# Optimization experiments

Hardware: AMD Instinct MI355X
Metric: run time of the kernel (lower is better)

Reference implementation:

```python
import jax, jax.numpy as jnp
import numpy as np

PATCH_SIZES = [4, 8, 12, 24]
SEQ_LEN = 336
D_MODEL = 512
BATCH = 256
N_EXPERTS = 4


def _build_gates():
    """Balanced top-2 routing: sample b -> experts (b%E, (b+1)%E). NNZ=512, 128 per expert."""
    rng = np.random.default_rng(0)
    gates = np.zeros((BATCH, N_EXPERTS), np.float32)
    for b in range(BATCH):
        e1, e2 = b % N_EXPERTS, (b + 1) % N_EXPERTS
        g = rng.uniform(0.1, 1.0, size=2).astype(np.float32)
        g = g / g.sum()
        gates[b, e1] = g[0]
        gates[b, e2] = g[1]
    nz = np.argwhere(gates > 0)                       # [NNZ, 2], batch-major (row-major)
    order = np.argsort(nz[:, 1], kind='stable')       # stable sort by expert -> batch order within expert
    return gates, nz[order, 0].astype(np.int64), nz[order, 1].astype(np.int64)


def setup_inputs() -> dict:
    key = jax.random.key(0)
    gates_np, batch_index, expert_index = _build_gates()
    counts = [int((expert_index == i).sum()) for i in range(N_EXPERTS)]  # 128 each
    keys = jax.random.split(key, 16)
    inp = {}
    for i, p in enumerate(PATCH_SIZES):
        L = SEQ_LEN // p
        inp[f'xs{i}'] = jax.random.normal(keys[i], (counts[i], L, D_MODEL), jnp.float32)
        inp[f'W{i}'] = jax.random.normal(keys[4 + i], (p * D_MODEL, D_MODEL), jnp.float32) * 0.02
        inp[f'b{i}'] = jnp.zeros((p * D_MODEL,), jnp.float32)
    inp['gates'] = jnp.asarray(gates_np)
    inp['Wp'] = jax.random.normal(keys[8], (D_MODEL, D_MODEL), jnp.float32) * 0.02
    inp['bp'] = jnp.zeros((D_MODEL,), jnp.float32)
    inp['batch_index'] = jnp.asarray(batch_index)
    inp['expert_index'] = jnp.asarray(expert_index)
    return inp


def reference(xs0, xs1, xs2, xs3, gates, W0, b0, W1, b1, W2, b2, W3, b3, Wp, bp,
              batch_index, expert_index):
    xs = [xs0, xs1, xs2, xs3]
    Ws = [(W0, b0), (W1, b1), (W2, b2), (W3, b3)]
    outs = []
    for x, (W, b), p in zip(xs, Ws, PATCH_SIZES):
        h = jnp.einsum('nld,pd->nlp', x, W) + b       # [N_i, L_i, P*D]
        n, l, _ = h.shape
        h = h.reshape(n, l * p, D_MODEL)[:, :SEQ_LEN]  # [N_i, seq_len, D]
        outs.append(h)
    stitched = jnp.concatenate(outs, axis=0)           # [NNZ, seq_len, D], expert-major
    proj = jnp.einsum('nld,ed->nle', stitched, Wp) + bp
    nonzero_gates = gates[batch_index, expert_index]   # [NNZ]
    proj = proj * nonzero_gates[:, None, None]
    combined = jnp.zeros((gates.shape[0], SEQ_LEN, D_MODEL), proj.dtype)
    combined = combined.at[batch_index].add(proj)      # gated scatter-combine
    return combined
```

## Files before the change

kernel.cpp:

```cpp
#include <hip/hip_runtime.h>
#include <stdint.h>

typedef __bf16 bf16_t;
typedef bf16_t bf16x8 __attribute__((ext_vector_type(8)));
typedef float f32x4 __attribute__((ext_vector_type(4)));
typedef unsigned short u16x8 __attribute__((ext_vector_type(8)));

#define KDIM 512

__device__ __forceinline__ unsigned short f2bf(float f) {
  unsigned int u = __float_as_uint(f);
  u = (u + 0x7FFFu + ((u >> 16) & 1u)) >> 16;
  return (unsigned short)u;
}

struct PrepArgs {
  const float *s0, *s1, *s2, *s3, *s4;
  unsigned short *d0, *d1, *d2, *d3, *d4;
  const float *w0, *w1, *w2, *w3;
  unsigned short *t0, *t1, *t2, *t3;
  const float *b0, *b1, *b2, *b3;
  const float *Wp, *bp;
  float *bf;
};
__device__ __forceinline__ void cvt8(const float* s, unsigned short* d, int i) {
  const float4* sp = (const float4*)s;
  float4 a = sp[2 * (size_t)i], b = sp[2 * (size_t)i + 1];
  u16x8 r;
  r[0] = f2bf(a.x); r[1] = f2bf(a.y); r[2] = f2bf(a.z); r[3] = f2bf(a.w);
  r[4] = f2bf(b.x); r[5] = f2bf(b.y); r[6] = f2bf(b.z); r[7] = f2bf(b.w);
  *(u16x8*)(d + (size_t)8 * i) = r;
}
__global__ __launch_bounds__(256) void prep_all(PrepArgs a) {
  __shared__ float tile[64][65];
  int bid = blockIdx.x;
  int t = threadIdx.x;
  if (bid < 48) {
    int jg = bid;
    int e, base;
    if (jg < 4)       { e = 0; base = 0; }
    else if (jg < 12) { e = 1; base = 4; }
    else if (jg < 24) { e = 2; base = 12; }
    else              { e = 3; base = 24; }
    const float* b = e == 0 ? a.b0 : e == 1 ? a.b1 : e == 2 ? a.b2 : a.b3;
    int jl = jg - base;
    const float4* br4 = (const float4*)(b + (size_t)jl * 512);
#pragma unroll
    for (int oo = 0; oo < 2; ++oo) {
      int o = t + oo * 256;
      const float4* wr4 = (const float4*)(a.Wp + (size_t)o * 512);
      float sx = 0.f, sy = 0.f, sz = 0.f, sw = 0.f;
#pragma unroll 4
      for (int i = 0; i < 128; ++i) {
        float4 wv = wr4[i], bv = br4[i];
        sx += wv.x * bv.x; sy += wv.y * bv.y; sz += wv.z * bv.z; sw += wv.w * bv.w;
      }
      a.bf[(size_t)jg * 512 + o] = a.bp[o] + ((sx + sy) + (sz + sw));
    }
  } else if (bid < 3120) {
    int r = bid - 48;
    int e, base, P;
    if (r < 256)       { e = 0; base = 0;    P = 4; }
    else if (r < 768)  { e = 1; base = 256;  P = 8; }
    else if (r < 1536) { e = 2; base = 768;  P = 12; }
    else               { e = 3; base = 1536; P = 24; }
    const float* W = e == 0 ? a.w0 : e == 1 ? a.w1 : e == 2 ? a.w2 : a.w3;
    unsigned short* Wt = e == 0 ? a.t0 : e == 1 ? a.t1 : e == 2 ? a.t2 : a.t3;
    r -= base;
    int qb = r % (P * 8), db = r / (P * 8);
    int q0 = qb * 64, d0 = db * 64;
    int c4 = t & 15, rgrp = t >> 4;
#pragma unroll
    for (int i = 0; i < 4; ++i) {
      int row = rgrp + i * 16;
      float4 v = *(const float4*)&W[(size_t)(q0 + row) * 512 + d0 + c4 * 4];
      tile[row][c4 * 4 + 0] = v.x; tile[row][c4 * 4 + 1] = v.y;
      tile[row][c4 * 4 + 2] = v.z; tile[row][c4 * 4 + 3] = v.w;
    }
    __syncthreads();
    int j = q0 >> 9, e0 = q0 & 511;
    size_t obase = (size_t)j * 262144 + (size_t)d0 * 512 + e0;
#pragma unroll
    for (int it = 0; it < 2; ++it) {
      int pair = it * 256 + t;
      int dd = pair >> 3, ch = pair & 7;
      u16x8 o8;
#pragma unroll
      for (int k = 0; k < 8; ++k) o8[k] = f2bf(tile[ch * 8 + k][dd]);
      *(u16x8*)&Wt[obase + (size_t)dd * 512 + ch * 8] = o8;
    }
  } else {
    int i = (bid - 3120) * 256 + t;
    if (i < 688128)       cvt8(a.s0, a.d0, i);
    else if (i < 1032192) cvt8(a.s1, a.d1, i - 688128);
    else if (i < 1261568) cvt8(a.s2, a.d2, i - 1032192);
    else if (i < 1376256) cvt8(a.s3, a.d3, i - 1261568);
    else                  cvt8(a.s4, a.d4, i - 1376256);
  }
}

__device__ __forceinline__ void gload_lds16(const unsigned short* g, unsigned short* l) {
  __builtin_amdgcn_global_load_lds(
      (const __attribute__((address_space(1))) void*)g,
      (__attribute__((address_space(3))) void*)l, 16, 0, 0);
}

__device__ __forceinline__ void stage32(const unsigned short* __restrict__ g,
                                        char* ldsOp, int tid, int kt) {
  int rlo = tid >> 2;
  int c = (tid & 3) ^ ((tid >> 3) & 3);
#pragma unroll
  for (int i = 0; i < 2; ++i) {
    int row = i * 64 + rlo;
    gload_lds16(g + (size_t)row * KDIM + kt * 32 + c * 8,
                (unsigned short*)(ldsOp + i * 4096 + tid * 16));
  }
}
__device__ __forceinline__ bf16x8 lds_frag32(const char* op, int r, int c16) {
  return *(const bf16x8*)(op + r * 64 + ((c16 ^ ((r >> 1) & 3)) << 4));
}

__device__ __forceinline__ void gemm128_k512(
    const unsigned short* __restrict__ Ag, const unsigned short* __restrict__ Bg,
    char* lds, int tid, f32x4 acc[4][4]) {
  int lane = tid & 63, w = tid >> 6;
  int wr0 = (w >> 1) * 64, wc0 = (w & 1) * 64;
  int c16 = lane >> 4, rl = lane & 15;
  stage32(Ag, lds, tid, 0);
  stage32(Bg, lds + 8192, tid, 0);
  stage32(Ag, lds + 16384, tid, 1);
  stage32(Bg, lds + 16384 + 8192, tid, 1);
#pragma unroll
  for (int s = 0; s < 16; ++s) {
    if (s < 15) asm volatile("s_waitcnt vmcnt(4)\n\ts_barrier" ::: "memory");
    else        asm volatile("s_waitcnt vmcnt(0)\n\ts_barrier" ::: "memory");
    char* cur = lds + (s % 3) * 16384;
    if (s + 2 < 16) {
      char* nxt = lds + ((s + 2) % 3) * 16384;
      stage32(Ag, nxt, tid, s + 2);
      stage32(Bg, nxt + 8192, tid, s + 2);
    }
    bf16x8 av[4], bv[4];
#pragma unroll
    for (int f = 0; f < 4; ++f) {
      av[f] = lds_frag32(cur, wr0 + f * 16 + rl, c16);
      bv[f] = lds_frag32(cur + 8192, wc0 + f * 16 + rl, c16);
    }
    __builtin_amdgcn_s_setprio(1);
#pragma unroll
    for (int fi = 0; fi < 4; ++fi)
#pragma unroll
      for (int fj = 0; fj < 4; ++fj)
        acc[fi][fj] = __builtin_amdgcn_mfma_f32_16x16x32_bf16(av[fi], bv[fj], acc[fi][fj], 0, 0, 0);
    __builtin_amdgcn_s_setprio(0);
  }
}

struct FuseArgs {
  const unsigned short *wt0, *wt1, *wt2, *wt3;
  unsigned short *wf0, *wf1, *wf2, *wf3;
};
__global__ __launch_bounds__(256, 3) void fuse_all(const unsigned short* __restrict__ Wpb, FuseArgs a) {
  __shared__ __align__(16) char lds[49152];
  int bid = blockIdx.x;
  int e, base, P;
  if (bid < 64)       { e = 0; base = 0;   P = 4; }
  else if (bid < 192) { e = 1; base = 64;  P = 8; }
  else if (bid < 384) { e = 2; base = 192; P = 12; }
  else                { e = 3; base = 384; P = 24; }
  const unsigned short* WtB = e == 0 ? a.wt0 : e == 1 ? a.wt1 : e == 2 ? a.wt2 : a.wt3;
  unsigned short* Wf = e == 0 ? a.wf0 : e == 1 ? a.wf1 : e == 2 ? a.wf2 : a.wf3;
  int r = bid - base;
  int tileM = r % (4 * P), tileN = r / (4 * P);
  int tid = threadIdx.x;
  int lane = tid & 63, w = tid >> 6;
  int wr0 = (w >> 1) * 64, wc0 = (w & 1) * 64;
  int j = (tileM * 128) >> 9;
  const unsigned short* Ag = Wpb + (size_t)((tileM * 128) & 511) * 512;
  const unsigned short* Bg = WtB + (size_t)j * 262144 + (size_t)(tileN * 128) * 512;
  f32x4 acc[4][4] = {};
  gemm128_k512(Ag, Bg, lds, tid, acc);
#pragma unroll
  for (int fi = 0; fi < 4; ++fi)
#pragma unroll
    for (int fj = 0; fj < 4; ++fj) {
      int col = tileN * 128 + wc0 + fj * 16 + (lane & 15);
#pragma unroll
      for (int r2 = 0; r2 < 4; ++r2) {
        int m = tileM * 128 + wr0 + fi * 16 + (lane >> 4) * 4 + r2;
        Wf[(size_t)m * 512 + col] = f2bf(acc[fi][fj][r2]);
      }
    }
}

template <int L, int P, int EXPERT, bool SLICE_M, bool STORE>
__device__ __forceinline__ void expert_body(
    const unsigned short* __restrict__ A, const unsigned short* __restrict__ Wf,
    const float* __restrict__ bf, const float* __restrict__ gates,
    const int* __restrict__ bidx, float* __restrict__ out, char* lds, int bid, int tid) {
  constexpr int TM = L;
  constexpr int TN = 4 * P;
  constexpr int EBASE = 128 * EXPERT;
  int xcd = bid & 7, pos = bid >> 3;
  int lin = xcd * (TM * TN / 8) + pos;
  int tileM, tileN;
  if (SLICE_M) { tileM = lin / TN; tileN = lin % TN; }
  else         { tileN = lin / TM; tileM = lin % TM; }

  int lane = tid & 63, w = tid >> 6;
  int wr0 = (w >> 1) * 64, wc0 = (w & 1) * 64;
  const unsigned short* Ag = A + (size_t)tileM * 128 * KDIM;
  const unsigned short* Bg = Wf + (size_t)tileN * 128 * KDIM;
  f32x4 acc[4][4] = {};
  gemm128_k512(Ag, Bg, lds, tid, acc);

  int j = tileN >> 2;
  int obase = (tileN & 3) * 128;
  float bv[4];
  int ocol[4];
#pragma unroll
  for (int fj = 0; fj < 4; ++fj) {
    ocol[fj] = obase + wc0 + fj * 16 + (lane & 15);
    bv[fj] = bf[(j << 9) + ocol[fj]];
  }
#pragma unroll
  for (int fi = 0; fi < 4; ++fi) {
    int m0 = tileM * 128 + wr0 + fi * 16 + (lane >> 4) * 4;
    int n = m0 / L, li = m0 - n * L;
    float* rp[4]; float gg[4];
#pragma unroll
    for (int r = 0; r < 4; ++r) {
      if (li == L) { li = 0; ++n; }
      int b = bidx[EBASE + n];
      gg[r] = gates[b * 4 + EXPERT];
      rp[r] = out + ((size_t)b * 336 + li * P + j) * 512;
      ++li;
    }
    float old[4][4];
    if (!STORE) {
#pragma unroll
      for (int r = 0; r < 4; ++r)
#pragma unroll
        for (int fj = 0; fj < 4; ++fj) old[r][fj] = rp[r][ocol[fj]];
    }
#pragma unroll
    for (int r = 0; r < 4; ++r)
#pragma unroll
      for (int fj = 0; fj < 4; ++fj) {
        float v = gg[r] * (acc[fi][fj][r] + bv[fj]);
        if (!STORE) v += old[r][fj];
        rp[r][ocol[fj]] = v;
      }
  }
}

struct ScatterArgs {
  const unsigned short *xa, *wa;
  const unsigned short *xb, *wb;
  const float *bfa, *bfb;
  const float *gates;
  const int *bidx;
  float *out;
};

__global__ __launch_bounds__(256, 3) void scatter_store(ScatterArgs a) {
  __shared__ __align__(16) char lds[49152];
  int tid = threadIdx.x;
  if (blockIdx.x < 1344)
    expert_body<84, 4, 0, true, true>(a.xa, a.wa, a.bfa, a.gates, a.bidx, a.out, lds, blockIdx.x, tid);
  else
    expert_body<28, 12, 2, false, true>(a.xb, a.wb, a.bfb, a.gates, a.bidx, a.out, lds, blockIdx.x - 1344, tid);
}

__global__ __launch_bounds__(256, 3) void scatter_add(ScatterArgs a) {
  __shared__ __align__(16) char lds[49152];
  int tid = threadIdx.x;
  if (blockIdx.x < 1344)
    expert_body<42, 8, 1, true, false>(a.xa, a.wa, a.bfa, a.gates, a.bidx, a.out, lds, blockIdx.x, tid);
  else
    expert_body<14, 24, 3, false, false>(a.xb, a.wb, a.bfb, a.gates, a.bidx, a.out, lds, blockIdx.x - 1344, tid);
}

extern "C" void kernel_launch(void* const* d_in, const int* in_sizes, int n_in,
                              void* d_out, int out_size, void* d_ws, size_t ws_size,
                              hipStream_t stream) {
  const float* xs[4]   = {(const float*)d_in[0], (const float*)d_in[3], (const float*)d_in[6], (const float*)d_in[9]};
  const float* Wfp[4]  = {(const float*)d_in[1], (const float*)d_in[4], (const float*)d_in[7], (const float*)d_in[10]};
  const float* bias[4] = {(const float*)d_in[2], (const float*)d_in[5], (const float*)d_in[8], (const float*)d_in[11]};
  const float* gates = (const float*)d_in[12];
  const float* Wp    = (const float*)d_in[13];
  const float* bp    = (const float*)d_in[14];
  const int* bidx    = (const int*)d_in[15];

  static const int xs_elems[4] = {5505024, 2752512, 1835008, 917504};
  static const int W_elems[4]  = {1048576, 2097152, 3145728, 6291456};

  unsigned short* w = (unsigned short*)d_ws;
  size_t off = 0;
  unsigned short* xsb[4]; unsigned short* WtB[4]; unsigned short* Wfb[4];
  for (int i = 0; i < 4; i++) { xsb[i] = w + off; off += xs_elems[i]; }
  for (int i = 0; i < 4; i++) { WtB[i] = w + off; off += W_elems[i]; }
  for (int i = 0; i < 4; i++) { Wfb[i] = w + off; off += W_elems[i]; }
  unsigned short* Wpb = w + off; off += 262144;
  float* bfused = (float*)(w + off);

  PrepArgs pa;
  pa.s0 = xs[0]; pa.s1 = xs[1]; pa.s2 = xs[2]; pa.s3 = xs[3]; pa.s4 = Wp;
  pa.d0 = xsb[0]; pa.d1 = xsb[1]; pa.d2 = xsb[2]; pa.d3 = xsb[3]; pa.d4 = Wpb;
  pa.w0 = Wfp[0]; pa.w1 = Wfp[1]; pa.w2 = Wfp[2]; pa.w3 = Wfp[3];
  pa.t0 = WtB[0]; pa.t1 = WtB[1]; pa.t2 = WtB[2]; pa.t3 = WtB[3];
  pa.b0 = bias[0]; pa.b1 = bias[1]; pa.b2 = bias[2]; pa.b3 = bias[3];
  pa.Wp = Wp; pa.bp = bp; pa.bf = bfused;
  prep_all<<<8624, 256, 0, stream>>>(pa);

  FuseArgs fa = {WtB[0], WtB[1], WtB[2], WtB[3], Wfb[0], Wfb[1], Wfb[2], Wfb[3]};
  fuse_all<<<768, 256, 0, stream>>>(Wpb, fa);

  ScatterArgs sa;
  sa.gates = gates; sa.bidx = bidx; sa.out = (float*)d_out;
  sa.xa = xsb[0]; sa.wa = Wfb[0]; sa.bfa = bfused + 0 * 512;
  sa.xb = xsb[2]; sa.wb = Wfb[2]; sa.bfb = bfused + 12 * 512;
  scatter_store<<<2688, 256, 0, stream>>>(sa);

  sa.xa = xsb[1]; sa.wa = Wfb[1]; sa.bfa = bfused + 4 * 512;
  sa.xb = xsb[3]; sa.wb = Wfb[3]; sa.bfb = bfused + 24 * 512;
  scatter_add<<<2688, 256, 0, stream>>>(sa);
}
```

Baseline: 230.4 us.

## Prefetch scatter-add accumulators before GEMM, use nontemporal stores and 2D XCD tiling

```diff
diff --git a/kernel.cpp b/kernel.cpp
--- a/kernel.cpp
+++ b/kernel.cpp
@@ -193,64 +193,73 @@
     }
 }
 
-template <int L, int P, int EXPERT, bool SLICE_M, bool STORE>
+template <int L, int P, int EXPERT, int XM, int XN, bool STORE>
 __device__ __forceinline__ void expert_body(
     const unsigned short* __restrict__ A, const unsigned short* __restrict__ Wf,
     const float* __restrict__ bf, const float* __restrict__ gates,
     const int* __restrict__ bidx, float* __restrict__ out, char* lds, int bid, int tid) {
   constexpr int TM = L;
   constexpr int TN = 4 * P;
+  constexpr int TMl = TM / XM, TNl = TN / XN;
   constexpr int EBASE = 128 * EXPERT;
   int xcd = bid & 7, pos = bid >> 3;
-  int lin = xcd * (TM * TN / 8) + pos;
-  int tileM, tileN;
-  if (SLICE_M) { tileM = lin / TN; tileN = lin % TN; }
-  else         { tileN = lin / TM; tileM = lin % TM; }
+  int tileM = (xcd / XN) * TMl + pos / TNl;
+  int tileN = (xcd % XN) * TNl + pos % TNl;
 
   int lane = tid & 63, w = tid >> 6;
   int wr0 = (w >> 1) * 64, wc0 = (w & 1) * 64;
   const unsigned short* Ag = A + (size_t)tileM * 128 * KDIM;
   const unsigned short* Bg = Wf + (size_t)tileN * 128 * KDIM;
+
+  int j = tileN >> 2;
+  int obase = (tileN & 3) * 128;
+  int ocol[4];
+#pragma unroll
+  for (int fj = 0; fj < 4; ++fj) ocol[fj] = obase + wc0 + fj * 16 + (lane & 15);
+
+  float old[4][4][4];
+  if (!STORE) {
+#pragma unroll
+    for (int fi = 0; fi < 4; ++fi) {
+      int m0 = tileM * 128 + wr0 + fi * 16 + (lane >> 4) * 4;
+      int n = m0 / L, li = m0 - n * L;
+#pragma unroll
+      for (int r = 0; r < 4; ++r) {
+        if (li == L) { li = 0; ++n; }
+        int b = bidx[EBASE + n];
+        const float* rp = out + ((size_t)b * 336 + li * P + j) * 512;
+#pragma unroll
+        for (int fj = 0; fj < 4; ++fj)
+          old[fi][r][fj] = __builtin_nontemporal_load(rp + ocol[fj]);
+        ++li;
+      }
+    }
+  }
+
   f32x4 acc[4][4] = {};
   gemm128_k512(Ag, Bg, lds, tid, acc);
 
-  int j = tileN >> 2;
-  int obase = (tileN & 3) * 128;
   float bv[4];
-  int ocol[4];
-#pragma unroll
-  for (int fj = 0; fj < 4; ++fj) {
-    ocol[fj] = obase + wc0 + fj * 16 + (lane & 15);
-    bv[fj] = bf[(j << 9) + ocol[fj]];
-  }
+#pragma unroll
+  for (int fj = 0; fj < 4; ++fj) bv[fj] = bf[(j << 9) + ocol[fj]];
 #pragma unroll
   for (int fi = 0; fi < 4; ++fi) {
     int m0 = tileM * 128 + wr0 + fi * 16 + (lane >> 4) * 4;
     int n = m0 / L, li = m0 - n * L;
-    float* rp[4]; float gg[4];
 #pragma unroll
     for (int r = 0; r < 4; ++r) {
       if (li == L) { li = 0; ++n; }
       int b = bidx[EBASE + n];
-      gg[r] = gates[b * 4 + EXPERT];
-      rp[r] = out + ((size_t)b * 336 + li * P + j) * 512;
+      float g = gates[b * 4 + EXPERT];
+      float* rp = out + ((size_t)b * 336 + li * P + j) * 512;
+#pragma unroll
+      for (int fj = 0; fj < 4; ++fj) {
+        float v = g * (acc[fi][fj][r] + bv[fj]);
+        if (!STORE) v += old[fi][r][fj];
+        __builtin_nontemporal_store(v, rp + ocol[fj]);
+      }
       ++li;
     }
-    float old[4][4];
-    if (!STORE) {
-#pragma unroll
-      for (int r = 0; r < 4; ++r)
-#pragma unroll
-        for (int fj = 0; fj < 4; ++fj) old[r][fj] = rp[r][ocol[fj]];
-    }
-#pragma unroll
-    for (int r = 0; r < 4; ++r)
-#pragma unroll
-      for (int fj = 0; fj < 4; ++fj) {
-        float v = gg[r] * (acc[fi][fj][r] + bv[fj]);
-        if (!STORE) v += old[r][fj];
-        rp[r][ocol[fj]] = v;
-      }
   }
 }
 
@@ -267,18 +276,18 @@
   __shared__ __align__(16) char lds[49152];
   int tid = threadIdx.x;
   if (blockIdx.x < 1344)
-    expert_body<84, 4, 0, true, true>(a.xa, a.wa, a.bfa, a.gates, a.bidx, a.out, lds, blockIdx.x, tid);
+    expert_body<84, 4, 0, 4, 2, true>(a.xa, a.wa, a.bfa, a.gates, a.bidx, a.out, lds, blockIdx.x, tid);
   else
-    expert_body<28, 12, 2, false, true>(a.xb, a.wb, a.bfb, a.gates, a.bidx, a.out, lds, blockIdx.x - 1344, tid);
+    expert_body<28, 12, 2, 2, 4, true>(a.xb, a.wb, a.bfb, a.gates, a.bidx, a.out, lds, blockIdx.x - 1344, tid);
 }
 
 __global__ __launch_bounds__(256, 3) void scatter_add(ScatterArgs a) {
   __shared__ __align__(16) char lds[49152];
   int tid = threadIdx.x;
   if (blockIdx.x < 1344)
-    expert_body<42, 8, 1, true, false>(a.xa, a.wa, a.bfa, a.gates, a.bidx, a.out, lds, blockIdx.x, tid);
+    expert_body<42, 8, 1, 2, 4, false>(a.xa, a.wa, a.bfa, a.gates, a.bidx, a.out, lds, blockIdx.x, tid);
   else
-    expert_body<14, 24, 3, false, false>(a.xb, a.wb, a.bfb, a.gates, a.bidx, a.out, lds, blockIdx.x - 1344, tid);
+    expert_body<14, 24, 3, 1, 8, false>(a.xb, a.wb, a.bfb, a.gates, a.bidx, a.out, lds, blockIdx.x - 1344, tid);
 }
 
 extern "C" void kernel_launch(void* const* d_in, const int* in_sizes, int n_in,
```

Result: slower. 363.5 us (+57.7%).
